# Performance work log

Measured on AMD Instinct MI355X. Metric: run time of the kernel, lower is better.

## Reference

```python
import jax, jax.numpy as jnp
import numpy as np

N = 50000      # nodes
E = 800000     # edges (avg degree 16)
IN = 512       # input features
OUT = 32       # per-head hidden features
H = 8          # heads (layer 1)
C = 16         # classes (layer 2, 1 head)
NEG_SLOPE = 0.2


def setup_inputs() -> dict:
    key = jax.random.key(0)
    ks = jax.random.split(key, 8)
    x = jax.random.normal(ks[0], (N, IN), jnp.float32)
    edge_index = jax.random.randint(ks[1], (2, E), 0, N, jnp.int32)
    # layer 1 params: W1 [IN, H*OUT], attention vectors a1_src/a1_dst [H, OUT]
    W1 = jax.random.normal(ks[2], (IN, H * OUT), jnp.float32) * (1.0 / np.sqrt(IN))
    a1_src = jax.random.normal(ks[3], (H, OUT), jnp.float32) * (1.0 / np.sqrt(OUT))
    a1_dst = jax.random.normal(ks[4], (H, OUT), jnp.float32) * (1.0 / np.sqrt(OUT))
    # layer 2 params: single head, W2 [H*OUT, C], a2_src/a2_dst [1, C]
    W2 = jax.random.normal(ks[5], (H * OUT, C), jnp.float32) * (1.0 / np.sqrt(H * OUT))
    a2_src = jax.random.normal(ks[6], (1, C), jnp.float32) * (1.0 / np.sqrt(C))
    a2_dst = jax.random.normal(ks[7], (1, C), jnp.float32) * (1.0 / np.sqrt(C))
    return {"x": x, "W1": W1, "a1_src": a1_src, "a1_dst": a1_dst,
            "W2": W2, "a2_src": a2_src, "a2_dst": a2_dst,
            "edge_index": edge_index}


def gat_layer(x, edge_index, W, a_src, a_dst, concat):
    """Standard GAT layer: e_ij = LeakyReLU(a_src.Wh_i + a_dst.Wh_j),
    softmax over incoming edges of each target node, scatter-aggregate."""
    n = x.shape[0]
    h_heads, f = a_src.shape
    h = (x @ W).reshape(n, h_heads, f)                      # [N, H, F]
    src, dst = edge_index[0], edge_index[1]
    es = jnp.einsum('nhf,hf->nh', h, a_src)                 # [N, H] per-node src scores
    ed = jnp.einsum('nhf,hf->nh', h, a_dst)                 # [N, H]
    e = jax.nn.leaky_relu(es[src] + ed[dst], NEG_SLOPE)     # [E, H] per-edge logits
    # segment softmax over edges grouped by dst node
    m = jax.ops.segment_max(e, dst, num_segments=n)         # [N, H]
    m = jnp.where(jnp.isfinite(m), m, 0.0)                  # empty segments -> -inf
    p = jnp.exp(e - m[dst])                                 # [E, H]
    s = jax.ops.segment_sum(p, dst, num_segments=n)         # [N, H]
    denom = s[dst]
    alpha = p / jnp.where(denom > 0, denom, 1.0)            # [E, H]
    msg = h[src] * alpha[:, :, None]                        # [E, H, F]
    out = jax.ops.segment_sum(msg, dst, num_segments=n)     # [N, H, F]
    if concat:
        return out.reshape(n, h_heads * f)
    return out.mean(axis=1)


def reference(x, W1, a1_src, a1_dst, W2, a2_src, a2_dst, edge_index):
    # dropout is identity in eval mode
    h = gat_layer(x, edge_index, W1, a1_src, a1_dst, concat=True)   # [N, H*OUT]
    h = jax.nn.elu(h)
    h = gat_layer(h, edge_index, W2, a2_src, a2_dst, concat=False)  # [N, C]
    return jax.nn.log_softmax(h, axis=1)
```

## Files before the change

kernel.cpp:

```cpp
#include <hip/hip_runtime.h>

#define NN 50000
#define EE 800000
#define KIN 512
#define HF 256
#define NH 8
#define FOUT 32
#define NC 16
#define NEG 0.2f
#define NB_SCAN 196

typedef unsigned short u16;
typedef __attribute__((ext_vector_type(8))) short shortx8;
typedef __attribute__((ext_vector_type(4))) float floatx4;
typedef __attribute__((ext_vector_type(8))) unsigned short ushortx8;
typedef __attribute__((ext_vector_type(4))) unsigned short ushortx4;

__device__ __forceinline__ float lrelu(float x) { return x > 0.f ? x : NEG * x; }

__device__ __forceinline__ u16 f2bf(float f) {
    unsigned u = __float_as_uint(f);
    return (u16)((u + 0x7FFFu + ((u >> 16) & 1u)) >> 16);
}
__device__ __forceinline__ float bf2f(u16 v) {
    return __uint_as_float((unsigned)v << 16);
}

__device__ __forceinline__ void gll16(const void* g, void* l) {
    __builtin_amdgcn_global_load_lds((const __attribute__((address_space(1))) void*)g,
                                     (__attribute__((address_space(3))) void*)l, 16, 0, 0);
}

__global__ void count_deg(const int* __restrict__ dst, int* __restrict__ deg) {
    int e = blockIdx.x * 256 + threadIdx.x;
    if (e < EE) atomicAdd(&deg[dst[e]], 1);
}

__global__ __launch_bounds__(256) void scan_a(const int* __restrict__ deg, int* __restrict__ bsum) {
    __shared__ int sm[256];
    int t = threadIdx.x;
    int i = blockIdx.x * 256 + t;
    sm[t] = (i < NN) ? deg[i] : 0;
    __syncthreads();
    for (int o = 128; o; o >>= 1) { if (t < o) sm[t] += sm[t + o]; __syncthreads(); }
    if (t == 0) bsum[blockIdx.x] = sm[0];
}

__global__ __launch_bounds__(256) void scan_b(const int* __restrict__ bsum, int* __restrict__ boff) {
    __shared__ int sm[256];
    int t = threadIdx.x;
    sm[t] = (t < NB_SCAN) ? bsum[t] : 0;
    __syncthreads();
    for (int d = 1; d < 256; d <<= 1) {
        int v = (t >= d) ? sm[t - d] : 0;
        __syncthreads();
        sm[t] += v;
        __syncthreads();
    }
    if (t < NB_SCAN) boff[t] = (t == 0) ? 0 : sm[t - 1];
}

__global__ __launch_bounds__(256) void scan_c(const int* __restrict__ deg, const int* __restrict__ boff,
                                              int* __restrict__ off) {
    __shared__ int sm[256];
    int t = threadIdx.x;
    int i = blockIdx.x * 256 + t;
    int d = (i < NN) ? deg[i] : 0;
    sm[t] = d;
    __syncthreads();
    for (int dd = 1; dd < 256; dd <<= 1) {
        int v = (t >= dd) ? sm[t - dd] : 0;
        __syncthreads();
        sm[t] += v;
        __syncthreads();
    }
    if (i < NN) off[i] = boff[blockIdx.x] + sm[t] - d;
    if (i == 0) off[NN] = EE;
}

__global__ void fill_csr(const int* __restrict__ src, const int* __restrict__ dst,
                         const int* __restrict__ off, int* __restrict__ cursor,
                         int* __restrict__ csr_src) {
    int e = blockIdx.x * 256 + threadIdx.x;
    if (e < EE) {
        int d = dst[e];
        int pos = atomicAdd(&cursor[d], 1);
        csr_src[off[d] + pos] = src[e];
    }
}

__global__ __launch_bounds__(256) void convert_x(const float* __restrict__ x, u16* __restrict__ xb) {
    size_t i = ((size_t)blockIdx.x * 256 + threadIdx.x) * 8;
    if (i >= (size_t)NN * KIN) return;
    float4 f0 = *(const float4*)(x + i);
    float4 f1 = *(const float4*)(x + i + 4);
    ushortx8 o;
    o[0] = f2bf(f0.x); o[1] = f2bf(f0.y); o[2] = f2bf(f0.z); o[3] = f2bf(f0.w);
    o[4] = f2bf(f1.x); o[5] = f2bf(f1.y); o[6] = f2bf(f1.z); o[7] = f2bf(f1.w);
    *(ushortx8*)(xb + i) = o;
}

__global__ __launch_bounds__(256) void convert_w1t(const float* __restrict__ W1, u16* __restrict__ w1t) {
    int e = blockIdx.x * 256 + threadIdx.x;
    int k = e >> 8, n = e & 255;
    w1t[n * KIN + k] = f2bf(W1[e]);
}

__global__ __launch_bounds__(256) void convert_w2t(const float* __restrict__ W2, u16* __restrict__ w2t) {
    int e = blockIdx.x * 256 + threadIdx.x;
    int k = e >> 4, c = e & 15;
    w2t[c * HF + k] = f2bf(W2[e]);
}

__global__ __launch_bounds__(256) void gemm1_mfma(const u16* __restrict__ xb,
                                                  const u16* __restrict__ w1t,
                                                  u16* __restrict__ h1b) {
    __shared__ __align__(16) u16 As[128 * 32];
    __shared__ __align__(16) u16 Bs[128 * 32];
    int t = threadIdx.x;
    int lane = t & 63, wave = t >> 6;
    int wm = wave >> 1, wn = wave & 1;
    int lm = lane & 15, quad = lane >> 4;
    int bm = blockIdx.x * 128;
    int bn = blockIdx.y * 128;

    floatx4 acc[4][4];
#pragma unroll
    for (int i = 0; i < 4; i++)
#pragma unroll
        for (int j = 0; j < 4; j++) acc[i][j] = (floatx4){0.f, 0.f, 0.f, 0.f};

    int sr = wave * 32 + (lane >> 2);
    int sk = (lane & 3) * 8;
    int ar0 = bm + sr, ar1 = ar0 + 16;
    if (ar0 > NN - 1) ar0 = NN - 1;
    if (ar1 > NN - 1) ar1 = NN - 1;
    const u16* agp0 = xb + (size_t)ar0 * KIN + sk;
    const u16* agp1 = xb + (size_t)ar1 * KIN + sk;
    const u16* bgp0 = w1t + (size_t)(bn + sr) * KIN + sk;
    const u16* bgp1 = w1t + (size_t)(bn + sr + 16) * KIN + sk;
    u16* asl0 = As + wave * 1024;
    u16* asl1 = As + wave * 1024 + 512;
    u16* bsl0 = Bs + wave * 1024;
    u16* bsl1 = Bs + wave * 1024 + 512;

    int offA[4], offB[4];
#pragma unroll
    for (int i = 0; i < 4; i++) offA[i] = (wm * 64 + i * 16 + lm) * 32 + quad * 8;
#pragma unroll
    for (int j = 0; j < 4; j++) offB[j] = (wn * 64 + j * 16 + lm) * 32 + quad * 8;

    for (int kk = 0; kk < KIN; kk += 32) {
        gll16(agp0 + kk, asl0);
        gll16(agp1 + kk, asl1);
        gll16(bgp0 + kk, bsl0);
        gll16(bgp1 + kk, bsl1);
        __syncthreads();
        shortx8 af[4], bf[4];
#pragma unroll
        for (int i = 0; i < 4; i++) af[i] = *(const shortx8*)&As[offA[i]];
#pragma unroll
        for (int j = 0; j < 4; j++) bf[j] = *(const shortx8*)&Bs[offB[j]];
#pragma unroll
        for (int i = 0; i < 4; i++)
#pragma unroll
            for (int j = 0; j < 4; j++)
                acc[i][j] = __builtin_amdgcn_mfma_f32_16x16x32_bf16(af[i], bf[j], acc[i][j], 0, 0, 0);
        __syncthreads();
    }

#pragma unroll
    for (int i = 0; i < 4; i++) {
        int row = bm + wm * 64 + i * 16 + quad * 4;
#pragma unroll
        for (int j = 0; j < 4; j++) {
            int col = bn + wn * 64 + j * 16 + lm;
#pragma unroll
            for (int r = 0; r < 4; r++) {
                if (row + r < NN) h1b[(size_t)(row + r) * HF + col] = f2bf(acc[i][j][r]);
            }
        }
    }
}

__global__ __launch_bounds__(256) void scores1(const u16* __restrict__ h1b, const float* __restrict__ a_src,
                                               const float* __restrict__ a_dst,
                                               float* __restrict__ es, float* __restrict__ ed) {
    __shared__ float as_s[HF], ad_s[HF];
    int t = threadIdx.x;
    as_s[t] = a_src[t];
    ad_s[t] = a_dst[t];
    __syncthreads();
    int nl = t >> 5;
    int L = t & 31;
    int n = blockIdx.x * 8 + nl;
    ushortx8 hv = *(const ushortx8*)(h1b + (size_t)n * HF + L * 8);
    float ps = 0.f, pd = 0.f;
#pragma unroll
    for (int i = 0; i < 8; i++) {
        float v = bf2f(hv[i]);
        ps += v * as_s[L * 8 + i];
        pd += v * ad_s[L * 8 + i];
    }
    ps += __shfl_down(ps, 2, 4); ps += __shfl_down(ps, 1, 4);
    pd += __shfl_down(pd, 2, 4); pd += __shfl_down(pd, 1, 4);
    if ((L & 3) == 0) {
        int h = L >> 2;
        es[n * NH + h] = ps;
        ed[n * NH + h] = pd;
    }
}

__global__ __launch_bounds__(256) void agg1(const u16* __restrict__ h1b, const float* __restrict__ es,
                                            const float* __restrict__ ed, const int* __restrict__ off,
                                            const int* __restrict__ csr_src, u16* __restrict__ out1b) {
    int n = blockIdx.x, t = threadIdx.x;
    __shared__ float edl[NH];
    __shared__ float p_chunk[32][9];
    __shared__ float sc_h[NH], s_h[NH];
    __shared__ int src_chunk[32];
    __shared__ float red[4][HF];
    int beg = off[n];
    int deg = off[n + 1] - beg;
    if (t < NH) edl[t] = ed[n * NH + t];
    int ph = t >> 5, el = t & 31;
    int w = t >> 6, L = t & 63;
    int ah = L >> 3;
    float m_run = -3.0e38f, s_run = 0.f;
    float acc0 = 0.f, acc1 = 0.f, acc2 = 0.f, acc3 = 0.f;
    __syncthreads();
    float edh = edl[ph];
    for (int base = 0; base < deg; base += 32) {
        int nch = deg - base; if (nch > 32) nch = 32;
        if (t < nch) src_chunk[t] = csr_src[beg + base + t];
        __syncthreads();
        float v = -3.0e38f;
        if (el < nch) v = lrelu(es[src_chunk[el] * NH + ph] + edh);
        float cm = v;
#pragma unroll
        for (int o = 16; o; o >>= 1) cm = fmaxf(cm, __shfl_down(cm, o, 32));
        cm = __shfl(cm, 0, 32);
        float m_new = fmaxf(m_run, cm);
        float sc = __expf(m_run - m_new);
        float p = (el < nch) ? __expf(v - m_new) : 0.f;
        float ps = p;
#pragma unroll
        for (int o = 16; o; o >>= 1) ps += __shfl_down(ps, o, 32);
        ps = __shfl(ps, 0, 32);
        s_run = s_run * sc + ps;
        m_run = m_new;
        p_chunk[el][ph] = p;
        if (el == 0) sc_h[ph] = sc;
        __syncthreads();
        float scl = sc_h[ah];
        acc0 *= scl; acc1 *= scl; acc2 *= scl; acc3 *= scl;
        for (int e = w; e < nch; e += 4) {
            float p2 = p_chunk[e][ah];
            ushortx4 hv = *(const ushortx4*)(h1b + (size_t)src_chunk[e] * HF + L * 4);
            acc0 += p2 * bf2f(hv[0]);
            acc1 += p2 * bf2f(hv[1]);
            acc2 += p2 * bf2f(hv[2]);
            acc3 += p2 * bf2f(hv[3]);
        }
        __syncthreads();
    }
    if (el == 0) s_h[ph] = s_run;
    *(float4*)&red[w][L * 4] = make_float4(acc0, acc1, acc2, acc3);
    __syncthreads();
    float vv = red[0][t] + red[1][t] + red[2][t] + red[3][t];
    float sh = s_h[t >> 5];
    vv *= (sh > 0.f ? 1.0f / sh : 0.f);
    out1b[(size_t)n * HF + t] = f2bf(vv > 0.f ? vv : (__expf(vv) - 1.0f));
}

__global__ __launch_bounds__(64) void gemm2_mfma(const u16* __restrict__ out1b, const u16* __restrict__ w2t,
                                                 const float* __restrict__ a2s, const float* __restrict__ a2d,
                                                 float* __restrict__ h2, float* __restrict__ es2,
                                                 float* __restrict__ ed2) {
    int lane = threadIdx.x;
    int lm = lane & 15, quad = lane >> 4;
    int nb = blockIdx.x * 16;
    floatx4 acc = (floatx4){0.f, 0.f, 0.f, 0.f};
    const u16* arow = out1b + (size_t)(nb + lm) * HF + quad * 8;
    const u16* brow = w2t + lm * HF + quad * 8;
#pragma unroll
    for (int kk = 0; kk < HF; kk += 32) {
        shortx8 af = *(const shortx8*)(arow + kk);
        shortx8 bf = *(const shortx8*)(brow + kk);
        acc = __builtin_amdgcn_mfma_f32_16x16x32_bf16(af, bf, acc, 0, 0, 0);
    }
    float a2sc = a2s[lm], a2dc = a2d[lm];
#pragma unroll
    for (int r = 0; r < 4; r++) {
        int n = nb + quad * 4 + r;
        float v = acc[r];
        h2[n * NC + lm] = v;
        float ps = v * a2sc, pd = v * a2dc;
#pragma unroll
        for (int o = 8; o; o >>= 1) {
            ps += __shfl_down(ps, o, 16);
            pd += __shfl_down(pd, o, 16);
        }
        if (lm == 0) { es2[n] = ps; ed2[n] = pd; }
    }
}

__global__ __launch_bounds__(256) void agg2(const float* __restrict__ h2, const float* __restrict__ es2,
                                            const float* __restrict__ ed2, const int* __restrict__ off,
                                            const int* __restrict__ csr_src, float* __restrict__ out) {
    int t = threadIdx.x;
    int nid = blockIdx.x * 16 + (t >> 4);
    int c = t & 15;
    int beg = off[nid];
    int deg = off[nid + 1] - beg;
    float edn = ed2[nid];
    float m = -3.0e38f, s = 0.f, acc = 0.f;
    for (int base = 0; base < deg; base += 16) {
        int nch = deg - base; if (nch > 16) nch = 16;
        int sv = 0; float ev = -3.0e38f;
        if (c < nch) {
            sv = csr_src[beg + base + c];
            ev = lrelu(es2[sv] + edn);
        }
        float cm = ev;
#pragma unroll
        for (int o = 8; o; o >>= 1) cm = fmaxf(cm, __shfl_down(cm, o, 16));
        cm = __shfl(cm, 0, 16);
        float mn = fmaxf(m, cm);
        float scl = __expf(m - mn);
        float p = (c < nch) ? __expf(ev - mn) : 0.f;
        float psum = p;
#pragma unroll
        for (int o = 8; o; o >>= 1) psum += __shfl_down(psum, o, 16);
        psum = __shfl(psum, 0, 16);
        s = s * scl + psum;
        acc *= scl;
        m = mn;
        for (int e = 0; e < nch; e++) {
            int sve = __shfl(sv, e, 16);
            float pe = __shfl(p, e, 16);
            acc += pe * h2[sve * NC + c];
        }
    }
    float v = (s > 0.f) ? acc / s : 0.f;
    float m2 = v;
#pragma unroll
    for (int o = 8; o; o >>= 1) m2 = fmaxf(m2, __shfl_down(m2, o, 16));
    m2 = __shfl(m2, 0, 16);
    float se = __expf(v - m2);
#pragma unroll
    for (int o = 8; o; o >>= 1) se += __shfl_down(se, o, 16);
    se = __shfl(se, 0, 16);
    out[nid * NC + c] = v - m2 - __logf(se);
}

extern "C" void kernel_launch(void* const* d_in, const int* in_sizes, int n_in,
                              void* d_out, int out_size, void* d_ws, size_t ws_size,
                              hipStream_t stream) {
    const float* x   = (const float*)d_in[0];
    const float* W1  = (const float*)d_in[1];
    const float* a1s = (const float*)d_in[2];
    const float* a1d = (const float*)d_in[3];
    const float* W2  = (const float*)d_in[4];
    const float* a2s = (const float*)d_in[5];
    const float* a2d = (const float*)d_in[6];
    const int*   ei  = (const int*)d_in[7];
    const int* srcv = ei;
    const int* dstv = ei + EE;
    float* out = (float*)d_out;

    u16* h1b   = (u16*)d_ws;
    u16* xb    = h1b + (size_t)NN * HF;
    u16* out1b = xb;
    float* es1 = (float*)(xb + (size_t)NN * KIN);
    float* ed1 = es1 + (size_t)NN * NH;
    float* h2  = ed1 + (size_t)NN * NH;
    u16* w1t   = (u16*)h2;
    float* es2v = h2 + (size_t)NN * NC;
    float* ed2v = es2v + NN;
    int* deg    = (int*)(ed2v + NN);
    int* cursor = deg + NN;
    int* offs   = cursor + NN;
    int* csr    = offs + NN + 1;
    int* bsum   = csr + EE;
    int* boff   = bsum + 256;
    u16* w2t    = (u16*)(boff + 256);

    hipMemsetAsync(deg, 0, NN * sizeof(int), stream);
    hipMemsetAsync(cursor, 0, NN * sizeof(int), stream);
    count_deg<<<(EE + 255) / 256, 256, 0, stream>>>(dstv, deg);
    scan_a<<<NB_SCAN, 256, 0, stream>>>(deg, bsum);
    scan_b<<<1, 256, 0, stream>>>(bsum, boff);
    scan_c<<<NB_SCAN, 256, 0, stream>>>(deg, boff, offs);
    fill_csr<<<(EE + 255) / 256, 256, 0, stream>>>(srcv, dstv, offs, cursor, csr);
    convert_x<<<((size_t)NN * KIN / 8 + 255) / 256, 256, 0, stream>>>(x, xb);
    convert_w1t<<<(KIN * HF) / 256, 256, 0, stream>>>(W1, w1t);
    convert_w2t<<<(HF * NC) / 256, 256, 0, stream>>>(W2, w2t);
    gemm1_mfma<<<dim3((NN + 127) / 128, HF / 128), 256, 0, stream>>>(xb, w1t, h1b);
    scores1<<<NN / 8, 256, 0, stream>>>(h1b, a1s, a1d, es1, ed1);
    agg1<<<NN, 256, 0, stream>>>(h1b, es1, ed1, offs, csr, out1b);
    gemm2_mfma<<<NN / 16, 64, 0, stream>>>(out1b, w2t, a2s, a2d, h2, es2v, ed2v);
    agg2<<<NN / 16, 256, 0, stream>>>(h2, es2v, ed2v, offs, csr, out);
}
```

Before: 433.0 us.

## Drop online-softmax max tracking and batch neighbor feature loads in aggregation kernels

Both aggregation kernels stop tracking a running maximum and rescaling, and instead accumulate exp(logit) directly and normalise by the summed weights at the end. The neighbor feature gathers are hoisted ahead of the softmax weight computation into register arrays, so up to 8 (layer 1) or 16 (layer 2) loads are in flight at once. This removes shuffle reductions, an exp for rescaling and one barrier per chunk. Without max subtraction it relies on the logits staying small enough not to overflow exp, and it uses more registers.

```diff
diff --git a/kernel.cpp b/kernel.cpp
--- a/kernel.cpp
+++ b/kernel.cpp
@@ -217,7 +217,7 @@
     int n = blockIdx.x, t = threadIdx.x;
     __shared__ float edl[NH];
     __shared__ float p_chunk[32][9];
-    __shared__ float sc_h[NH], s_h[NH];
+    __shared__ float s_h[NH];
     __shared__ int src_chunk[32];
     __shared__ float red[4][HF];
     int beg = off[n];
@@ -226,7 +226,7 @@
     int ph = t >> 5, el = t & 31;
     int w = t >> 6, L = t & 63;
     int ah = L >> 3;
-    float m_run = -3.0e38f, s_run = 0.f;
+    float s_part = 0.f;
     float acc0 = 0.f, acc1 = 0.f, acc2 = 0.f, acc3 = 0.f;
     __syncthreads();
     float edh = edl[ph];
@@ -234,37 +234,33 @@
         int nch = deg - base; if (nch > 32) nch = 32;
         if (t < nch) src_chunk[t] = csr_src[beg + base + t];
         __syncthreads();
-        float v = -3.0e38f;
-        if (el < nch) v = lrelu(es[src_chunk[el] * NH + ph] + edh);
-        float cm = v;
-#pragma unroll
-        for (int o = 16; o; o >>= 1) cm = fmaxf(cm, __shfl_down(cm, o, 32));
-        cm = __shfl(cm, 0, 32);
-        float m_new = fmaxf(m_run, cm);
-        float sc = __expf(m_run - m_new);
-        float p = (el < nch) ? __expf(v - m_new) : 0.f;
-        float ps = p;
-#pragma unroll
-        for (int o = 16; o; o >>= 1) ps += __shfl_down(ps, o, 32);
-        ps = __shfl(ps, 0, 32);
-        s_run = s_run * sc + ps;
-        m_run = m_new;
+        ushortx4 hv[8];
+#pragma unroll
+        for (int i = 0; i < 8; i++) {
+            int e = w + i * 4;
+            if (e < nch) hv[i] = *(const ushortx4*)(h1b + (size_t)src_chunk[e] * HF + L * 4);
+        }
+        float p = 0.f;
+        if (el < nch) p = __expf(lrelu(es[src_chunk[el] * NH + ph] + edh));
+        s_part += p;
         p_chunk[el][ph] = p;
-        if (el == 0) sc_h[ph] = sc;
-        __syncthreads();
-        float scl = sc_h[ah];
-        acc0 *= scl; acc1 *= scl; acc2 *= scl; acc3 *= scl;
-        for (int e = w; e < nch; e += 4) {
-            float p2 = p_chunk[e][ah];
-            ushortx4 hv = *(const ushortx4*)(h1b + (size_t)src_chunk[e] * HF + L * 4);
-            acc0 += p2 * bf2f(hv[0]);
-            acc1 += p2 * bf2f(hv[1]);
-            acc2 += p2 * bf2f(hv[2]);
-            acc3 += p2 * bf2f(hv[3]);
+        __syncthreads();
+#pragma unroll
+        for (int i = 0; i < 8; i++) {
+            int e = w + i * 4;
+            if (e < nch) {
+                float p2 = p_chunk[e][ah];
+                acc0 += p2 * bf2f(hv[i][0]);
+                acc1 += p2 * bf2f(hv[i][1]);
+                acc2 += p2 * bf2f(hv[i][2]);
+                acc3 += p2 * bf2f(hv[i][3]);
+            }
         }
         __syncthreads();
     }
-    if (el == 0) s_h[ph] = s_run;
+#pragma unroll
+    for (int o = 16; o; o >>= 1) s_part += __shfl_down(s_part, o, 32);
+    if (el == 0) s_h[ph] = s_part;
     *(float4*)&red[w][L * 4] = make_float4(acc0, acc1, acc2, acc3);
     __syncthreads();
     float vv = red[0][t] + red[1][t] + red[2][t] + red[3][t];
@@ -314,34 +310,29 @@
     int beg = off[nid];
     int deg = off[nid + 1] - beg;
     float edn = ed2[nid];
-    float m = -3.0e38f, s = 0.f, acc = 0.f;
+    float s = 0.f, acc = 0.f;
     for (int base = 0; base < deg; base += 16) {
         int nch = deg - base; if (nch > 16) nch = 16;
-        int sv = 0; float ev = -3.0e38f;
-        if (c < nch) {
-            sv = csr_src[beg + base + c];
-            ev = lrelu(es2[sv] + edn);
-        }
-        float cm = ev;
-#pragma unroll
-        for (int o = 8; o; o >>= 1) cm = fmaxf(cm, __shfl_down(cm, o, 16));
-        cm = __shfl(cm, 0, 16);
-        float mn = fmaxf(m, cm);
-        float scl = __expf(m - mn);
-        float p = (c < nch) ? __expf(ev - mn) : 0.f;
-        float psum = p;
-#pragma unroll
-        for (int o = 8; o; o >>= 1) psum += __shfl_down(psum, o, 16);
-        psum = __shfl(psum, 0, 16);
-        s = s * scl + psum;
-        acc *= scl;
-        m = mn;
-        for (int e = 0; e < nch; e++) {
-            int sve = __shfl(sv, e, 16);
-            float pe = __shfl(p, e, 16);
-            acc += pe * h2[sve * NC + c];
-        }
-    }
+        int sv = 0;
+        if (c < nch) sv = csr_src[beg + base + c];
+        int sva[16];
+#pragma unroll
+        for (int e = 0; e < 16; e++) sva[e] = __shfl(sv, e, 16);
+        float hva[16];
+#pragma unroll
+        for (int e = 0; e < 16; e++) hva[e] = h2[sva[e] * NC + c];
+        float p = 0.f;
+        if (c < nch) p = __expf(lrelu(es2[sv] + edn));
+        s += p;
+        float pa[16];
+#pragma unroll
+        for (int e = 0; e < 16; e++) pa[e] = __shfl(p, e, 16);
+#pragma unroll
+        for (int e = 0; e < 16; e++) acc += pa[e] * hva[e];
+    }
+#pragma unroll
+    for (int o = 8; o; o >>= 1) s += __shfl_down(s, o, 16);
+    s = __shfl(s, 0, 16);
     float v = (s > 0.f) ? acc / s : 0.f;
     float m2 = v;
 #pragma unroll
```

New measurement: 424.6 us. About the same (-1.9%).
